# Kernel optimization log

Measured on AMD Instinct MI355X. Metric: run time of the kernel, lower is better.

## Reference

```python
import jax, jax.numpy as jnp
import numpy as np

L, B = 1024, 64
VALID_FRAC = 0.9  # fraction of residues with nonzero (observed) coordinates in y


def setup_inputs() -> dict:
    key = jax.random.key(0)
    kx, ky = jax.random.split(key)
    x = jax.random.normal(kx, (L, B, 3), dtype=jnp.float32)
    y = jax.random.normal(ky, (L, B, 3), dtype=jnp.float32)
    # zero out trailing residues in y so the dynamic mask (co.sum() != 0) is exercised
    valid = (jnp.arange(L) < int(VALID_FRAC * L))[:, None, None]
    y = y * valid.astype(jnp.float32)
    return {"x": x, "y": y}


def _masked_pair_dist(pts, pair_mask):
    # pts: [B, L, 3]; pair_mask: [B, L, L] (False on diagonal and on padded rows/cols)
    sq = jnp.sum(pts * pts, axis=-1)                                   # [B, L]
    d2 = sq[:, :, None] + sq[:, None, :] - 2.0 * jnp.einsum('bld,bmd->blm', pts, pts)
    d2 = jnp.maximum(d2, 0.0)                                          # relu, matches F.relu
    safe = jnp.where(pair_mask, d2, 1.0)                               # keep sqrt grad finite
    return jnp.where(pair_mask, jnp.sqrt(safe), 0.0)


def reference(x, y):
    # x, y: [L, B, 3] -> permute to [B, L, 3] as in the torch module
    xb = jnp.transpose(x, (1, 0, 2))
    yb = jnp.transpose(y, (1, 0, 2))
    Bn, Ln = xb.shape[0], xb.shape[1]
    # mask: residues of y whose coordinate sum is nonzero (index_select in original)
    mask = (jnp.sum(yb, axis=-1) != 0)                                 # [B, L]
    off_diag = ~jnp.eye(Ln, dtype=bool)
    pair_mask = mask[:, :, None] & mask[:, None, :] & off_diag         # [B, L, L]
    xd = _masked_pair_dist(xb, pair_mask)
    yd = _masked_pair_dist(yb, pair_mask)
    D = yd - xd                                                        # [B, L, L]
    per_batch = jnp.sqrt(jnp.sum(D * D, axis=(1, 2)))                  # Frobenius norm per batch
    denom = (Ln ** 2 / 2 - Ln) ** 0.5                                  # x.size(1)**2/2 - x.size(1)
    out = jnp.sum(per_batch) / denom / Bn
    return out.reshape(1)
```

## Files before the change

kernel.cpp:

```cpp
#include <hip/hip_runtime.h>
#include <math.h>

#define Lp 1024
#define Bp 64
#define Tt 128
#define NTILE 8
#define NPAIR 36

typedef float v2 __attribute__((ext_vector_type(2)));
static __device__ __forceinline__ v2 splat2(float s) { v2 r; r.x = s; r.y = s; return r; }
static __device__ __forceinline__ v2 lo2(float4 v)   { v2 r; r.x = v.x; r.y = v.y; return r; }
static __device__ __forceinline__ v2 hi2(float4 v)   { v2 r; r.x = v.z; r.y = v.w; return r; }

__global__ __launch_bounds__(256) void drmsd_main(
    const float* __restrict__ x, const float* __restrict__ y,
    float* __restrict__ partials, float* __restrict__ moments)
{
    __shared__ __align__(16) float xsx[2][Tt], xsy[2][Tt], xsz[2][Tt];
    __shared__ __align__(16) float ysx[2][Tt], ysy[2][Tt], ysz[2][Tt];
    __shared__ __align__(16) float ms[2][Tt];
    __shared__ float red[4];
    __shared__ float mred[4][9];

    const int b = blockIdx.x;
    const int p = blockIdx.y;
    const int t = threadIdx.x;

    if (p == NPAIR) {
        float v[9];
#pragma unroll
        for (int k = 0; k < 9; ++k) v[k] = 0.0f;
#pragma unroll
        for (int k = 0; k < 4; ++k) {
            const int row = t + k * 256;
            const float* px = x + (size_t)row * (Bp * 3) + (size_t)b * 3;
            const float* py = y + (size_t)row * (Bp * 3) + (size_t)b * 3;
            const float x0 = px[0], x1 = px[1], x2 = px[2];
            const float y0 = py[0], y1 = py[1], y2 = py[2];
            const float m = ((y0 + y1 + y2) != 0.0f) ? 1.0f : 0.0f;
            v[0] += m * x0; v[1] += m * x1; v[2] += m * x2;
            v[3] = fmaf(m, fmaf(x0, x0, fmaf(x1, x1, x2 * x2)), v[3]);
            v[4] += m * y0; v[5] += m * y1; v[6] += m * y2;
            v[7] = fmaf(m, fmaf(y0, y0, fmaf(y1, y1, y2 * y2)), v[7]);
            v[8] += m;
        }
#pragma unroll
        for (int k = 0; k < 9; ++k) {
#pragma unroll
            for (int off = 32; off > 0; off >>= 1)
                v[k] += __shfl_down(v[k], off, 64);
        }
        const int wave = t >> 6;
        if ((t & 63) == 0) {
#pragma unroll
            for (int k = 0; k < 9; ++k) mred[wave][k] = v[k];
        }
        __syncthreads();
        if (t < 9)
            moments[(size_t)b * 9 + t] =
                mred[0][t] + mred[1][t] + mred[2][t] + mred[3][t];
        return;
    }

    int ti = 0, base = 0;
    while (p >= base + (NTILE - ti)) { base += (NTILE - ti); ++ti; }
    const int tj = ti + (p - base);

    {
        const int r     = t & (Tt - 1);
        const int which = t >> 7;
        const int tile  = which ? tj : ti;
        const int row   = tile * Tt + r;
        const float* px = x + (size_t)row * (Bp * 3) + (size_t)b * 3;
        const float* py = y + (size_t)row * (Bp * 3) + (size_t)b * 3;
        const float x0 = px[0], x1 = px[1], x2 = px[2];
        const float y0 = py[0], y1 = py[1], y2 = py[2];
        xsx[which][r] = x0; xsy[which][r] = x1; xsz[which][r] = x2;
        ysx[which][r] = y0; ysy[which][r] = y1; ysz[which][r] = y2;
        ms[which][r]  = ((y0 + y1 + y2) != 0.0f) ? 1.0f : 0.0f;
    }
    __syncthreads();

    const int jc = (t & 15) << 2;
    const int rg = t >> 4;

    float total = 0.0f;

#pragma unroll
    for (int half = 0; half < 2; ++half) {
        const int i0 = half * 64 + rg * 4;
        const float4 v_xx = *(const float4*)&xsx[0][i0];
        const float4 v_xy = *(const float4*)&xsy[0][i0];
        const float4 v_xz = *(const float4*)&xsz[0][i0];
        const float4 v_yx = *(const float4*)&ysx[0][i0];
        const float4 v_yy = *(const float4*)&ysy[0][i0];
        const float4 v_yz = *(const float4*)&ysz[0][i0];
        const float4 v_mi = *(const float4*)&ms[0][i0];
        const float xix[4] = { v_xx.x, v_xx.y, v_xx.z, v_xx.w };
        const float xiy[4] = { v_xy.x, v_xy.y, v_xy.z, v_xy.w };
        const float xiz[4] = { v_xz.x, v_xz.y, v_xz.z, v_xz.w };
        const float yix[4] = { v_yx.x, v_yx.y, v_yx.z, v_yx.w };
        const float yiy[4] = { v_yy.x, v_yy.y, v_yy.z, v_yy.w };
        const float yiz[4] = { v_yz.x, v_yz.y, v_yz.z, v_yz.w };
        const float mir[4] = { v_mi.x, v_mi.y, v_mi.z, v_mi.w };

        v2 acc[4];
#pragma unroll
        for (int r = 0; r < 4; ++r) acc[r] = splat2(0.0f);

#pragma unroll
        for (int jj = 0; jj < 2; ++jj) {
            const int j0 = jj * 64 + jc;
            const float4 xjx4 = *(const float4*)&xsx[1][j0];
            const float4 xjy4 = *(const float4*)&xsy[1][j0];
            const float4 xjz4 = *(const float4*)&xsz[1][j0];
            const float4 yjx4 = *(const float4*)&ysx[1][j0];
            const float4 yjy4 = *(const float4*)&ysy[1][j0];
            const float4 yjz4 = *(const float4*)&ysz[1][j0];
            const float4 mj4  = *(const float4*)&ms[1][j0];
#pragma unroll
            for (int s = 0; s < 2; ++s) {
                const v2 xjx = s ? hi2(xjx4) : lo2(xjx4);
                const v2 xjy = s ? hi2(xjy4) : lo2(xjy4);
                const v2 xjz = s ? hi2(xjz4) : lo2(xjz4);
                const v2 yjx = s ? hi2(yjx4) : lo2(yjx4);
                const v2 yjy = s ? hi2(yjy4) : lo2(yjy4);
                const v2 yjz = s ? hi2(yjz4) : lo2(yjz4);
                const v2 mj  = s ? hi2(mj4)  : lo2(mj4);
#pragma unroll
                for (int r = 0; r < 4; ++r) {
                    const v2 ax = splat2(xix[r]) - xjx;
                    const v2 ay = splat2(xiy[r]) - xjy;
                    const v2 az = splat2(xiz[r]) - xjz;
                    const v2 d2x = ax * ax + ay * ay + az * az;
                    const v2 bx = splat2(yix[r]) - yjx;
                    const v2 by = splat2(yiy[r]) - yjy;
                    const v2 bz = splat2(yiz[r]) - yjz;
                    const v2 d2y = bx * bx + by * by + bz * bz;
                    const v2 pr = d2x * d2y;
                    v2 sq;
                    sq.x = __builtin_amdgcn_sqrtf(pr.x);
                    sq.y = __builtin_amdgcn_sqrtf(pr.y);
                    acc[r] = mj * sq + acc[r];
                }
            }
        }
#pragma unroll
        for (int r = 0; r < 4; ++r)
            total = fmaf(acc[r].x + acc[r].y, mir[r], total);
    }

#pragma unroll
    for (int off = 32; off > 0; off >>= 1)
        total += __shfl_down(total, off, 64);
    const int wave = t >> 6;
    if ((t & 63) == 0) red[wave] = total;
    __syncthreads();
    if (t == 0) {
        float s = red[0] + red[1] + red[2] + red[3];
        if (ti != tj) s *= 2.0f;
        partials[(size_t)p * Bp + b] = s;
    }
}

__global__ __launch_bounds__(64) void drmsd_final(
    const float* __restrict__ partials, const float* __restrict__ moments,
    float* __restrict__ out)
{
    const int b = threadIdx.x;
    double cross = 0.0;
#pragma unroll
    for (int pp = 0; pp < NPAIR; ++pp)
        cross += (double)partials[(size_t)pp * Bp + b];

    const float* mo = moments + (size_t)b * 9;
    const double sx0 = mo[0], sx1 = mo[1], sx2 = mo[2], qx = mo[3];
    const double sy0 = mo[4], sy1 = mo[5], sy2 = mo[6], qy = mo[7];
    const double M   = mo[8];
    const double term1 = 2.0 * M * (qx + qy)
        - 2.0 * (sx0*sx0 + sx1*sx1 + sx2*sx2 + sy0*sy0 + sy1*sy1 + sy2*sy2);

    double su = term1 - 2.0 * cross;
    su = su > 0.0 ? su : 0.0;
    double pb = sqrt(su);
#pragma unroll
    for (int off = 32; off > 0; off >>= 1)
        pb += __shfl_down(pb, off, 64);
    if (b == 0) {
        const double denom = sqrt((double)Lp * (double)Lp / 2.0 - (double)Lp);
        out[0] = (float)(pb / denom / (double)Bp);
    }
}

extern "C" void kernel_launch(void* const* d_in, const int* in_sizes, int n_in,
                              void* d_out, int out_size, void* d_ws, size_t ws_size,
                              hipStream_t stream) {
    const float* x = (const float*)d_in[0];
    const float* y = (const float*)d_in[1];
    float* out      = (float*)d_out;
    float* partials = (float*)d_ws;
    float* moments  = partials + NPAIR * Bp;

    dim3 grid(Bp, NPAIR + 1);
    drmsd_main<<<grid, 256, 0, stream>>>(x, y, partials, moments);
    drmsd_final<<<1, 64, 0, stream>>>(partials, moments, out);
}
```

Before: 69.32 us.

## Fold moment reduction into diagonal tile blocks and hoist j-tile LDS loads

```diff
diff --git a/kernel.cpp b/kernel.cpp
--- a/kernel.cpp
+++ b/kernel.cpp
@@ -25,42 +25,6 @@
     const int b = blockIdx.x;
     const int p = blockIdx.y;
     const int t = threadIdx.x;
-
-    if (p == NPAIR) {
-        float v[9];
-#pragma unroll
-        for (int k = 0; k < 9; ++k) v[k] = 0.0f;
-#pragma unroll
-        for (int k = 0; k < 4; ++k) {
-            const int row = t + k * 256;
-            const float* px = x + (size_t)row * (Bp * 3) + (size_t)b * 3;
-            const float* py = y + (size_t)row * (Bp * 3) + (size_t)b * 3;
-            const float x0 = px[0], x1 = px[1], x2 = px[2];
-            const float y0 = py[0], y1 = py[1], y2 = py[2];
-            const float m = ((y0 + y1 + y2) != 0.0f) ? 1.0f : 0.0f;
-            v[0] += m * x0; v[1] += m * x1; v[2] += m * x2;
-            v[3] = fmaf(m, fmaf(x0, x0, fmaf(x1, x1, x2 * x2)), v[3]);
-            v[4] += m * y0; v[5] += m * y1; v[6] += m * y2;
-            v[7] = fmaf(m, fmaf(y0, y0, fmaf(y1, y1, y2 * y2)), v[7]);
-            v[8] += m;
-        }
-#pragma unroll
-        for (int k = 0; k < 9; ++k) {
-#pragma unroll
-            for (int off = 32; off > 0; off >>= 1)
-                v[k] += __shfl_down(v[k], off, 64);
-        }
-        const int wave = t >> 6;
-        if ((t & 63) == 0) {
-#pragma unroll
-            for (int k = 0; k < 9; ++k) mred[wave][k] = v[k];
-        }
-        __syncthreads();
-        if (t < 9)
-            moments[(size_t)b * 9 + t] =
-                mred[0][t] + mred[1][t] + mred[2][t] + mred[3][t];
-        return;
-    }
 
     int ti = 0, base = 0;
     while (p >= base + (NTILE - ti)) { base += (NTILE - ti); ++ti; }
@@ -83,6 +47,19 @@
 
     const int jc = (t & 15) << 2;
     const int rg = t >> 4;
+
+    float4 jxx[2], jxy[2], jxz[2], jyx[2], jyy[2], jyz[2], jm4[2];
+#pragma unroll
+    for (int jj = 0; jj < 2; ++jj) {
+        const int j0 = jj * 64 + jc;
+        jxx[jj] = *(const float4*)&xsx[1][j0];
+        jxy[jj] = *(const float4*)&xsy[1][j0];
+        jxz[jj] = *(const float4*)&xsz[1][j0];
+        jyx[jj] = *(const float4*)&ysx[1][j0];
+        jyy[jj] = *(const float4*)&ysy[1][j0];
+        jyz[jj] = *(const float4*)&ysz[1][j0];
+        jm4[jj] = *(const float4*)&ms[1][j0];
+    }
 
     float total = 0.0f;
 
@@ -110,23 +87,15 @@
 
 #pragma unroll
         for (int jj = 0; jj < 2; ++jj) {
-            const int j0 = jj * 64 + jc;
-            const float4 xjx4 = *(const float4*)&xsx[1][j0];
-            const float4 xjy4 = *(const float4*)&xsy[1][j0];
-            const float4 xjz4 = *(const float4*)&xsz[1][j0];
-            const float4 yjx4 = *(const float4*)&ysx[1][j0];
-            const float4 yjy4 = *(const float4*)&ysy[1][j0];
-            const float4 yjz4 = *(const float4*)&ysz[1][j0];
-            const float4 mj4  = *(const float4*)&ms[1][j0];
 #pragma unroll
             for (int s = 0; s < 2; ++s) {
-                const v2 xjx = s ? hi2(xjx4) : lo2(xjx4);
-                const v2 xjy = s ? hi2(xjy4) : lo2(xjy4);
-                const v2 xjz = s ? hi2(xjz4) : lo2(xjz4);
-                const v2 yjx = s ? hi2(yjx4) : lo2(yjx4);
-                const v2 yjy = s ? hi2(yjy4) : lo2(yjy4);
-                const v2 yjz = s ? hi2(yjz4) : lo2(yjz4);
-                const v2 mj  = s ? hi2(mj4)  : lo2(mj4);
+                const v2 xjx = s ? hi2(jxx[jj]) : lo2(jxx[jj]);
+                const v2 xjy = s ? hi2(jxy[jj]) : lo2(jxy[jj]);
+                const v2 xjz = s ? hi2(jxz[jj]) : lo2(jxz[jj]);
+                const v2 yjx = s ? hi2(jyx[jj]) : lo2(jyx[jj]);
+                const v2 yjy = s ? hi2(jyy[jj]) : lo2(jyy[jj]);
+                const v2 yjz = s ? hi2(jyz[jj]) : lo2(jyz[jj]);
+                const v2 mj  = s ? hi2(jm4[jj]) : lo2(jm4[jj]);
 #pragma unroll
                 for (int r = 0; r < 4; ++r) {
                     const v2 ax = splat2(xix[r]) - xjx;
@@ -161,6 +130,36 @@
         if (ti != tj) s *= 2.0f;
         partials[(size_t)p * Bp + b] = s;
     }
+
+    if (ti == tj) {
+        float v[9];
+#pragma unroll
+        for (int k = 0; k < 9; ++k) v[k] = 0.0f;
+        if (t < Tt) {
+            const float x0 = xsx[0][t], x1 = xsy[0][t], x2 = xsz[0][t];
+            const float y0 = ysx[0][t], y1 = ysy[0][t], y2 = ysz[0][t];
+            const float m  = ms[0][t];
+            v[0] = m * x0; v[1] = m * x1; v[2] = m * x2;
+            v[3] = m * fmaf(x0, x0, fmaf(x1, x1, x2 * x2));
+            v[4] = m * y0; v[5] = m * y1; v[6] = m * y2;
+            v[7] = m * fmaf(y0, y0, fmaf(y1, y1, y2 * y2));
+            v[8] = m;
+        }
+#pragma unroll
+        for (int k = 0; k < 9; ++k) {
+#pragma unroll
+            for (int off = 32; off > 0; off >>= 1)
+                v[k] += __shfl_down(v[k], off, 64);
+        }
+        if ((t & 63) == 0) {
+#pragma unroll
+            for (int k = 0; k < 9; ++k) mred[wave][k] = v[k];
+        }
+        __syncthreads();
+        if (t < 9)
+            moments[(size_t)(ti * 9 + t) * Bp + b] =
+                mred[0][t] + mred[1][t] + mred[2][t] + mred[3][t];
+    }
 }
 
 __global__ __launch_bounds__(64) void drmsd_final(
@@ -173,7 +172,15 @@
     for (int pp = 0; pp < NPAIR; ++pp)
         cross += (double)partials[(size_t)pp * Bp + b];
 
-    const float* mo = moments + (size_t)b * 9;
+    double mo[9];
+#pragma unroll
+    for (int k = 0; k < 9; ++k) mo[k] = 0.0;
+#pragma unroll
+    for (int s = 0; s < NTILE; ++s) {
+#pragma unroll
+        for (int k = 0; k < 9; ++k)
+            mo[k] += (double)moments[(size_t)(s * 9 + k) * Bp + b];
+    }
     const double sx0 = mo[0], sx1 = mo[1], sx2 = mo[2], qx = mo[3];
     const double sy0 = mo[4], sy1 = mo[5], sy2 = mo[6], qy = mo[7];
     const double M   = mo[8];
@@ -201,7 +208,7 @@
     float* partials = (float*)d_ws;
     float* moments  = partials + NPAIR * Bp;
 
-    dim3 grid(Bp, NPAIR + 1);
+    dim3 grid(Bp, NPAIR);
     drmsd_main<<<grid, 256, 0, stream>>>(x, y, partials, moments);
     drmsd_final<<<1, 64, 0, stream>>>(partials, moments, out);
 }
```

New measurement: 71.62 us. 1.03x slower.
